# Kernel optimization log

Measured on AMD Instinct MI355X. Metric: run time of the kernel, lower is better.

The kernel has to match this reference:

```python
import jax, jax.numpy as jnp
import numpy as np
from jax import lax

B, D, H = 32768, 128, 256
N_ITER = 20


def setup_inputs() -> dict:
    key = jax.random.key(0)
    ks = jax.random.split(key, 7)
    return {
        "r": jax.random.normal(ks[0], (B, D), dtype=jnp.float32),
        "s": jax.random.normal(ks[1], (B, 1), dtype=jnp.float32),
        "pivot": jax.random.normal(ks[2], (D,), dtype=jnp.float32),
        "W1": jax.random.normal(ks[3], (D, H), dtype=jnp.float32) * 0.1,
        "b1": jax.random.normal(ks[4], (H,), dtype=jnp.float32) * 0.1,
        "w2": jax.random.normal(ks[5], (H,), dtype=jnp.float32) * 0.1,
        "b2": jax.random.normal(ks[6], (1,), dtype=jnp.float32) * 0.1,
        "n_iter": N_ITER,
    }


def _omega_step(x, W1, b1, w2, b2):
    # scalar implicit field omega evaluated on [B, D] points -> positive step in (0, 0.1)
    h = jnp.tanh(x @ W1 + b1)                      # [B, H]
    return 0.05 * (1.0 + jnp.tanh(h @ w2 + b2[0]))  # [B]


def reference(r, s, pivot, W1, b1, w2, b2, n_iter):
    # normalize ray directions; norm is detached in the original (stop_gradient)
    norm_of_x = jnp.linalg.norm(r, axis=1, keepdims=True)  # [B, 1]
    r_norm = r / lax.stop_gradient(norm_of_x)              # [B, D]

    # 20-step sphere-tracing-style ray marching along r_norm from pivot
    def step(alpha, _):
        x = pivot[None, :] + alpha[:, None] * r_norm       # [B, D]
        return alpha + _omega_step(x, W1, b1, w2, b2), None

    alpha0 = jnp.zeros((r.shape[0],), dtype=r.dtype)
    res_alpha, _ = lax.scan(step, alpha0, None, length=n_iter)  # [B]

    scale = jax.nn.sigmoid(s) * res_alpha[:, None]         # [B, 1]
    res_x = pivot[None, :] + scale * r_norm                # [B, D]
    return res_x
```

## Files before the change

### kernel.cpp

```cpp
#include <hip/hip_runtime.h>

#define DIM 128
#define HID 256
#define K2LE 2.885390081777927f
#define NTILES 16
#define RPB 32
#define BFPAD 136

typedef __attribute__((ext_vector_type(8))) short bf16x8;
typedef __attribute__((ext_vector_type(4))) float f32x4;

__device__ __forceinline__ unsigned short f2bf(float f) {
    union { float f; unsigned u; } x; x.f = f;
    unsigned r = x.u + 0x7fffu + ((x.u >> 16) & 1u);
    return (unsigned short)(r >> 16);
}

__device__ __forceinline__ float sigmoid_fast(float x) {
    float t = __builtin_amdgcn_exp2f(-x * 1.4426950408889634f);
    return __builtin_amdgcn_rcpf(1.0f + t);
}

__device__ __forceinline__ float row16_allreduce(float x) {
    int t;
    t = __builtin_amdgcn_update_dpp(0, __float_as_int(x), 0xB1, 0xf, 0xf, true);
    x += __int_as_float(t);
    t = __builtin_amdgcn_update_dpp(0, __float_as_int(x), 0x4E, 0xf, 0xf, true);
    x += __int_as_float(t);
    t = __builtin_amdgcn_update_dpp(0, __float_as_int(x), 0x124, 0xf, 0xf, true);
    x += __int_as_float(t);
    t = __builtin_amdgcn_update_dpp(0, __float_as_int(x), 0x128, 0xf, 0xf, true);
    x += __int_as_float(t);
    return x;
}

__global__ void k_prep(const float* __restrict__ pivot,
                       const float* __restrict__ W1,
                       const float* __restrict__ b1,
                       float* __restrict__ c2,
                       uint4* __restrict__ W1f) {
    const int tid = threadIdx.x;
    if (blockIdx.x == 0) {
        float a = b1[tid];
#pragma unroll 8
        for (int d = 0; d < DIM; ++d) a = fmaf(pivot[d], W1[d * HID + tid], a);
        c2[tid] = K2LE * a;
    }
    const int e  = blockIdx.x * 256 + tid;
    const int m  = e & 15;
    const int q  = (e >> 4) & 3;
    const int kk = (e >> 6) & 3;
    const int nt = e >> 8;
    const int n  = nt * 16 + m;
    const int k0 = kk * 32 + q * 8;
    unsigned w[4];
#pragma unroll
    for (int p = 0; p < 4; ++p) {
        unsigned lo = f2bf(W1[(k0 + 2 * p    ) * HID + n] * K2LE);
        unsigned hi = f2bf(W1[(k0 + 2 * p + 1) * HID + n] * K2LE);
        w[p] = lo | (hi << 16);
    }
    W1f[e] = make_uint4(w[0], w[1], w[2], w[3]);
}

__global__ __launch_bounds__(256, 4) void k_main(
    const float* __restrict__ r,
    const float* __restrict__ s,
    const float* __restrict__ pivot,
    const float* __restrict__ w2,
    const float* __restrict__ b2,
    const int* __restrict__ n_iter_p,
    const float* __restrict__ c2,
    const uint4* __restrict__ W1f,
    float* __restrict__ out)
{
    __shared__ unsigned short rnbf[RPB][BFPAD];
    __shared__ float rnf[RPB][DIM];
    __shared__ float alpha_s[RPB];

    const int tid  = threadIdx.x;
    const int lane = tid & 63;
    const int wave = tid >> 6;
    const int pr   = wave >> 1;
    const int par  = wave & 1;
    const int m    = lane & 15;
    const int q    = lane >> 4;
    const int rowblk = blockIdx.x * RPB;
    const int n_iter = *n_iter_p;

#pragma unroll
    for (int t = 0; t < 8; ++t) {
        const int lr = wave * 8 + t;
        float2 v = *(const float2*)&r[(rowblk + lr) * DIM + lane * 2];
        float ss = v.x * v.x + v.y * v.y;
#pragma unroll
        for (int msk = 32; msk >= 1; msk >>= 1) ss += __shfl_xor(ss, msk, 64);
        float inv = __builtin_amdgcn_rsqf(ss);
        float2 rn; rn.x = v.x * inv; rn.y = v.y * inv;
        *(float2*)&rnf[lr][lane * 2] = rn;
        unsigned pack = (unsigned)f2bf(rn.x) | ((unsigned)f2bf(rn.y) << 16);
        *(unsigned*)&rnbf[lr][lane * 2] = pack;
    }
    __syncthreads();

    bf16x8 afrag[4];
#pragma unroll
    for (int kk = 0; kk < 4; ++kk)
        afrag[kk] = *(const bf16x8*)&rnbf[pr * 16 + m][kk * 32 + q * 8];

    const bf16x8* __restrict__ wf = (const bf16x8*)W1f;
    const int fb = q * 16 + m;
    float gA[NTILES], gB[NTILES];
#pragma unroll
    for (int nt = 0; nt < NTILES; ++nt) {
        f32x4 a = {0.f, 0.f, 0.f, 0.f};
#pragma unroll
        for (int kk = 0; kk < 4; ++kk)
            a = __builtin_amdgcn_mfma_f32_16x16x32_bf16(
                    afrag[kk], wf[nt * 256 + kk * 64 + fb], a, 0, 0, 0);
        gA[nt] = a[par * 2 + 0];
        gB[nt] = a[par * 2 + 1];
    }

    float w2f[NTILES], c2f[NTILES];
#pragma unroll
    for (int nt = 0; nt < NTILES; ++nt) {
        w2f[nt] = w2[nt * 16 + m];
        c2f[nt] = c2[nt * 16 + m];
    }
    float S = 0.f;
#pragma unroll
    for (int nt = 0; nt < NTILES; ++nt) S += w2f[nt];
    S = row16_allreduce(S);
    const float C0 = K2LE * (S + b2[0]);

    float alphaA = 0.f, alphaB = 0.f;
    for (int it = 0; it < n_iter; ++it) {
        float pA = 0.f, pB = 0.f;
#pragma unroll
        for (int nt = 0; nt < NTILES; ++nt) {
            float uA = __builtin_amdgcn_rcpf(__builtin_amdgcn_exp2f(fmaf(alphaA, gA[nt], c2f[nt])) + 1.0f);
            float uB = __builtin_amdgcn_rcpf(__builtin_amdgcn_exp2f(fmaf(alphaB, gB[nt], c2f[nt])) + 1.0f);
            pA = fmaf(w2f[nt], uA, pA);
            pB = fmaf(w2f[nt], uB, pB);
        }
        pA = row16_allreduce(pA);
        pB = row16_allreduce(pB);
        float vA = __builtin_amdgcn_rcpf(__builtin_amdgcn_exp2f(fmaf(-2.0f * K2LE, pA, C0)) + 1.0f);
        float vB = __builtin_amdgcn_rcpf(__builtin_amdgcn_exp2f(fmaf(-2.0f * K2LE, pB, C0)) + 1.0f);
        alphaA += fmaf(-0.1f, vA, 0.1f);
        alphaB += fmaf(-0.1f, vB, 0.1f);
    }

    if (m == 0) {
        alpha_s[pr * 16 + q * 4 + par * 2 + 0] = alphaA;
        alpha_s[pr * 16 + q * 4 + par * 2 + 1] = alphaB;
    }
    __syncthreads();

    const float2 pv = *(const float2*)&pivot[lane * 2];
#pragma unroll
    for (int t = 0; t < 8; ++t) {
        const int lr  = wave * 8 + t;
        const int row = rowblk + lr;
        const float scale = sigmoid_fast(s[row]) * alpha_s[lr];
        float2 rn = *(const float2*)&rnf[lr][lane * 2];
        float2 o;
        o.x = fmaf(scale, rn.x, pv.x);
        o.y = fmaf(scale, rn.y, pv.y);
        *(float2*)&out[row * DIM + lane * 2] = o;
    }
}

extern "C" void kernel_launch(void* const* d_in, const int* in_sizes, int n_in,
                              void* d_out, int out_size, void* d_ws, size_t ws_size,
                              hipStream_t stream) {
    const float* r      = (const float*)d_in[0];
    const float* s      = (const float*)d_in[1];
    const float* pivot  = (const float*)d_in[2];
    const float* W1     = (const float*)d_in[3];
    const float* b1     = (const float*)d_in[4];
    const float* w2     = (const float*)d_in[5];
    const float* b2     = (const float*)d_in[6];
    const int*   n_iter = (const int*)d_in[7];
    float* out = (float*)d_out;

    float* c2  = (float*)d_ws;
    uint4* W1f = (uint4*)((char*)d_ws + 4096);

    const int B = in_sizes[0] / DIM;

    k_prep<<<16, 256, 0, stream>>>(pivot, W1, b1, c2, W1f);
    k_main<<<B / RPB, 256, 0, stream>>>(r, s, pivot, w2, b2, n_iter, c2, W1f, out);
}
```

Measured before the change: 131.1 us.

## Split fused kernel into GEMM and march kernels via bf16 workspace buffers

Splits the fused kernel into a GEMM kernel and a march kernel. The GEMM kernel computes the per-ray projection g = rn·W1 with MFMA and writes it to workspace as bf16, along with the normalized rays in bf16. The march kernel then runs the 20-iteration loop with one ray per 16 lanes and fewer registers, which allows higher occupancy (launch bounds 8). The aim is to stop the low-occupancy fused kernel from bottlenecking on transcendental latency. In exchange it adds about 24 MB of global traffic and two extra rounds of bf16 rounding: on g, and on the normalized direction used in the output. A fallback to the fused kernel is kept in case the workspace is too small.

```diff
diff --git a/kernel.cpp b/kernel.cpp
--- a/kernel.cpp
+++ b/kernel.cpp
@@ -4,7 +4,6 @@
 #define HID 256
 #define K2LE 2.885390081777927f
 #define NTILES 16
-#define RPB 32
 #define BFPAD 136
 
 typedef __attribute__((ext_vector_type(8))) short bf16x8;
@@ -15,6 +14,8 @@
     unsigned r = x.u + 0x7fffu + ((x.u >> 16) & 1u);
     return (unsigned short)(r >> 16);
 }
+__device__ __forceinline__ float bflo(unsigned u) { return __uint_as_float(u << 16); }
+__device__ __forceinline__ float bfhi(unsigned u) { return __uint_as_float(u & 0xffff0000u); }
 
 __device__ __forceinline__ float sigmoid_fast(float x) {
     float t = __builtin_amdgcn_exp2f(-x * 1.4426950408889634f);
@@ -37,14 +38,21 @@
 __global__ void k_prep(const float* __restrict__ pivot,
                        const float* __restrict__ W1,
                        const float* __restrict__ b1,
+                       const float* __restrict__ w2,
                        float* __restrict__ c2,
+                       float* __restrict__ c2p,
+                       float* __restrict__ w2p,
                        uint4* __restrict__ W1f) {
     const int tid = threadIdx.x;
     if (blockIdx.x == 0) {
         float a = b1[tid];
 #pragma unroll 8
         for (int d = 0; d < DIM; ++d) a = fmaf(pivot[d], W1[d * HID + tid], a);
-        c2[tid] = K2LE * a;
+        float cv = K2LE * a;
+        c2[tid] = cv;
+        const int pidx = (tid & 15) * 16 + (tid >> 4);
+        c2p[pidx] = cv;
+        w2p[pidx] = w2[tid];
     }
     const int e  = blockIdx.x * 256 + tid;
     const int m  = e & 15;
@@ -63,20 +71,148 @@
     W1f[e] = make_uint4(w[0], w[1], w[2], w[3]);
 }
 
-__global__ __launch_bounds__(256, 4) void k_main(
+__global__ __launch_bounds__(256, 4) void k_gemm(
     const float* __restrict__ r,
+    const uint4* __restrict__ W1f,
+    unsigned* __restrict__ rn_g,
+    uint4* __restrict__ g_buf)
+{
+    __shared__ unsigned short rnbf[64][BFPAD];
+
+    const int tid  = threadIdx.x;
+    const int lane = tid & 63;
+    const int wave = tid >> 6;
+    const int m    = lane & 15;
+    const int q    = lane >> 4;
+    const int rowb = blockIdx.x * 64 + wave * 16;
+
+#pragma unroll 4
+    for (int t = 0; t < 16; ++t) {
+        const int row = rowb + t;
+        float2 v = *(const float2*)&r[row * DIM + lane * 2];
+        float ss = v.x * v.x + v.y * v.y;
+#pragma unroll
+        for (int msk = 32; msk >= 1; msk >>= 1) ss += __shfl_xor(ss, msk, 64);
+        float inv = __builtin_amdgcn_rsqf(ss);
+        unsigned pack = (unsigned)f2bf(v.x * inv) | ((unsigned)f2bf(v.y * inv) << 16);
+        *(unsigned*)&rnbf[wave * 16 + t][lane * 2] = pack;
+        rn_g[row * 64 + lane] = pack;
+    }
+
+    bf16x8 afrag[4];
+#pragma unroll
+    for (int kk = 0; kk < 4; ++kk)
+        afrag[kk] = *(const bf16x8*)&rnbf[wave * 16 + m][kk * 32 + q * 8];
+
+    const bf16x8* __restrict__ wf = (const bf16x8*)W1f;
+    const int fb = q * 16 + m;
+    unsigned pk[4][8];
+#pragma unroll
+    for (int nt = 0; nt < NTILES; ++nt) {
+        f32x4 a = {0.f, 0.f, 0.f, 0.f};
+#pragma unroll
+        for (int kk = 0; kk < 4; ++kk)
+            a = __builtin_amdgcn_mfma_f32_16x16x32_bf16(
+                    afrag[kk], wf[nt * 256 + kk * 64 + fb], a, 0, 0, 0);
+#pragma unroll
+        for (int reg = 0; reg < 4; ++reg) {
+            unsigned h = f2bf(a[reg]);
+            if (nt & 1) pk[reg][nt >> 1] |= (h << 16);
+            else        pk[reg][nt >> 1]  = h;
+        }
+    }
+#pragma unroll
+    for (int reg = 0; reg < 4; ++reg) {
+        const int ray = rowb + q * 4 + reg;
+        uint4* p = g_buf + ray * 32 + m * 2;
+        p[0] = make_uint4(pk[reg][0], pk[reg][1], pk[reg][2], pk[reg][3]);
+        p[1] = make_uint4(pk[reg][4], pk[reg][5], pk[reg][6], pk[reg][7]);
+    }
+}
+
+__global__ __launch_bounds__(256, 8) void k_march(
+    const uint4* __restrict__ g_buf,
+    const uint4* __restrict__ rn_g,
     const float* __restrict__ s,
     const float* __restrict__ pivot,
-    const float* __restrict__ w2,
+    const float* __restrict__ c2p,
+    const float* __restrict__ w2p,
     const float* __restrict__ b2,
     const int* __restrict__ n_iter_p,
-    const float* __restrict__ c2,
-    const uint4* __restrict__ W1f,
     float* __restrict__ out)
 {
-    __shared__ unsigned short rnbf[RPB][BFPAD];
-    __shared__ float rnf[RPB][DIM];
-    __shared__ float alpha_s[RPB];
+    const int tid  = threadIdx.x;
+    const int lane = tid & 63;
+    const int wave = tid >> 6;
+    const int m    = lane & 15;
+    const int q    = lane >> 4;
+    const int ray  = blockIdx.x * 16 + wave * 4 + q;
+    const int n_iter = *n_iter_p;
+
+    uint4 ga = g_buf[ray * 32 + m * 2];
+    uint4 gb = g_buf[ray * 32 + m * 2 + 1];
+    float g[16];
+    g[0]=bflo(ga.x); g[1]=bfhi(ga.x); g[2]=bflo(ga.y); g[3]=bfhi(ga.y);
+    g[4]=bflo(ga.z); g[5]=bfhi(ga.z); g[6]=bflo(ga.w); g[7]=bfhi(ga.w);
+    g[8]=bflo(gb.x); g[9]=bfhi(gb.x); g[10]=bflo(gb.y); g[11]=bfhi(gb.y);
+    g[12]=bflo(gb.z); g[13]=bfhi(gb.z); g[14]=bflo(gb.w); g[15]=bfhi(gb.w);
+
+    float c[16], w[16];
+#pragma unroll
+    for (int i = 0; i < 4; ++i) {
+        float4 cv = *(const float4*)(c2p + m * 16 + i * 4);
+        float4 wv = *(const float4*)(w2p + m * 16 + i * 4);
+        c[4*i]=cv.x; c[4*i+1]=cv.y; c[4*i+2]=cv.z; c[4*i+3]=cv.w;
+        w[4*i]=wv.x; w[4*i+1]=wv.y; w[4*i+2]=wv.z; w[4*i+3]=wv.w;
+    }
+    float S = 0.f;
+#pragma unroll
+    for (int i = 0; i < 16; ++i) S += w[i];
+    S = row16_allreduce(S);
+    const float C0 = K2LE * (S + b2[0]);
+
+    float alpha = 0.f;
+    for (int it = 0; it < n_iter; ++it) {
+        float p = 0.f;
+#pragma unroll
+        for (int i = 0; i < 16; ++i) {
+            float u = __builtin_amdgcn_rcpf(
+                __builtin_amdgcn_exp2f(fmaf(alpha, g[i], c[i])) + 1.0f);
+            p = fmaf(w[i], u, p);
+        }
+        p = row16_allreduce(p);
+        float v = __builtin_amdgcn_rcpf(
+            __builtin_amdgcn_exp2f(fmaf(-2.0f * K2LE, p, C0)) + 1.0f);
+        alpha += fmaf(-0.1f, v, 0.1f);
+    }
+
+    const float sc = sigmoid_fast(s[ray]) * alpha;
+    uint4 rl = rn_g[ray * 16 + m];
+    float4 pv0 = *(const float4*)(pivot + m * 8);
+    float4 pv1 = *(const float4*)(pivot + m * 8 + 4);
+    float4 o0, o1;
+    o0.x = fmaf(sc, bflo(rl.x), pv0.x);
+    o0.y = fmaf(sc, bfhi(rl.x), pv0.y);
+    o0.z = fmaf(sc, bflo(rl.y), pv0.z);
+    o0.w = fmaf(sc, bfhi(rl.y), pv0.w);
+    o1.x = fmaf(sc, bflo(rl.z), pv1.x);
+    o1.y = fmaf(sc, bfhi(rl.z), pv1.y);
+    o1.z = fmaf(sc, bflo(rl.w), pv1.z);
+    o1.w = fmaf(sc, bfhi(rl.w), pv1.w);
+    *(float4*)(out + ray * DIM + m * 8)     = o0;
+    *(float4*)(out + ray * DIM + m * 8 + 4) = o1;
+}
+
+__global__ __launch_bounds__(256, 4) void k_main_fused(
+    const float* __restrict__ r, const float* __restrict__ s,
+    const float* __restrict__ pivot, const float* __restrict__ w2,
+    const float* __restrict__ b2, const int* __restrict__ n_iter_p,
+    const float* __restrict__ c2, const uint4* __restrict__ W1f,
+    float* __restrict__ out)
+{
+    __shared__ unsigned short rnbf[32][BFPAD];
+    __shared__ float rnf[32][DIM];
+    __shared__ float alpha_s[32];
 
     const int tid  = threadIdx.x;
     const int lane = tid & 63;
@@ -85,7 +221,7 @@
     const int par  = wave & 1;
     const int m    = lane & 15;
     const int q    = lane >> 4;
-    const int rowblk = blockIdx.x * RPB;
+    const int rowblk = blockIdx.x * 32;
     const int n_iter = *n_iter_p;
 
 #pragma unroll
@@ -121,7 +257,6 @@
         gA[nt] = a[par * 2 + 0];
         gB[nt] = a[par * 2 + 1];
     }
-
     float w2f[NTILES], c2f[NTILES];
 #pragma unroll
     for (int nt = 0; nt < NTILES; ++nt) {
@@ -151,7 +286,6 @@
         alphaA += fmaf(-0.1f, vA, 0.1f);
         alphaB += fmaf(-0.1f, vB, 0.1f);
     }
-
     if (m == 0) {
         alpha_s[pr * 16 + q * 4 + par * 2 + 0] = alphaA;
         alpha_s[pr * 16 + q * 4 + par * 2 + 1] = alphaB;
@@ -185,11 +319,25 @@
     const int*   n_iter = (const int*)d_in[7];
     float* out = (float*)d_out;
 
-    float* c2  = (float*)d_ws;
-    uint4* W1f = (uint4*)((char*)d_ws + 4096);
-
     const int B = in_sizes[0] / DIM;
 
-    k_prep<<<16, 256, 0, stream>>>(pivot, W1, b1, c2, W1f);
-    k_main<<<B / RPB, 256, 0, stream>>>(r, s, pivot, w2, b2, n_iter, c2, W1f, out);
-}
+    char* ws = (char*)d_ws;
+    float* c2   = (float*)(ws);
+    float* c2p  = (float*)(ws + 1024);
+    float* w2p  = (float*)(ws + 2048);
+    uint4* W1f  = (uint4*)(ws + 4096);
+    uint4* g_buf = (uint4*)(ws + 69632);
+    unsigned* rn_g = (unsigned*)(ws + 69632 + (size_t)B * 512);
+
+    const size_t need = 69632 + (size_t)B * 768;
+
+    k_prep<<<16, 256, 0, stream>>>(pivot, W1, b1, w2, c2, c2p, w2p, W1f);
+    if (ws_size >= need) {
+        k_gemm<<<B / 64, 256, 0, stream>>>(r, W1f, rn_g, g_buf);
+        k_march<<<B / 16, 256, 0, stream>>>(g_buf, (const uint4*)rn_g, s, pivot,
+                                            c2p, w2p, b2, n_iter, out);
+    } else {
+        k_main_fused<<<B / 32, 256, 0, stream>>>(r, s, pivot, w2, b2, n_iter,
+                                                 c2, W1f, out);
+    }
+}
```

Result: slower. 142.8 us (+8.9%).

## Split hidden-tile MFMA across waves and map one ray per 16-lane group

Applied to the files above, without the earlier changes.

Each block now handles 16 rays instead of 32. Each wave computes only 4 of the 16 hidden tiles of the projection with MFMA, and the waves exchange the results through shared memory, so the projection is no longer recomputed redundantly in every wave. In the march loop each 16-lane group owns one ray instead of each lane carrying two, which lowers register pressure and allows a launch bound of 8 blocks instead of 4. The c2/w2 constants are pre-permuted in the prep kernel so they can be read with vector loads. The fp32 normalized-ray copy is dropped and the output is rebuilt from bf16-rounded directions, which adds numerical error to the result.

```diff
diff --git a/kernel.cpp b/kernel.cpp
--- a/kernel.cpp
+++ b/kernel.cpp
@@ -4,8 +4,6 @@
 #define HID 256
 #define K2LE 2.885390081777927f
 #define NTILES 16
-#define RPB 32
-#define BFPAD 136
 
 typedef __attribute__((ext_vector_type(8))) short bf16x8;
 typedef __attribute__((ext_vector_type(4))) float f32x4;
@@ -15,6 +13,8 @@
     unsigned r = x.u + 0x7fffu + ((x.u >> 16) & 1u);
     return (unsigned short)(r >> 16);
 }
+__device__ __forceinline__ float bflo(unsigned u) { return __uint_as_float(u << 16); }
+__device__ __forceinline__ float bfhi(unsigned u) { return __uint_as_float(u & 0xffff0000u); }
 
 __device__ __forceinline__ float sigmoid_fast(float x) {
     float t = __builtin_amdgcn_exp2f(-x * 1.4426950408889634f);
@@ -37,14 +37,18 @@
 __global__ void k_prep(const float* __restrict__ pivot,
                        const float* __restrict__ W1,
                        const float* __restrict__ b1,
-                       float* __restrict__ c2,
+                       const float* __restrict__ w2,
+                       float* __restrict__ c2p,
+                       float* __restrict__ w2p,
                        uint4* __restrict__ W1f) {
     const int tid = threadIdx.x;
     if (blockIdx.x == 0) {
         float a = b1[tid];
 #pragma unroll 8
         for (int d = 0; d < DIM; ++d) a = fmaf(pivot[d], W1[d * HID + tid], a);
-        c2[tid] = K2LE * a;
+        const int pidx = (tid & 15) * 16 + (tid >> 4);
+        c2p[pidx] = K2LE * a;
+        w2p[pidx] = w2[tid];
     }
     const int e  = blockIdx.x * 256 + tid;
     const int m  = e & 15;
@@ -63,113 +67,109 @@
     W1f[e] = make_uint4(w[0], w[1], w[2], w[3]);
 }
 
-__global__ __launch_bounds__(256, 4) void k_main(
+__global__ __launch_bounds__(256, 8) void k_main(
     const float* __restrict__ r,
     const float* __restrict__ s,
     const float* __restrict__ pivot,
-    const float* __restrict__ w2,
+    const float* __restrict__ c2p,
+    const float* __restrict__ w2p,
     const float* __restrict__ b2,
     const int* __restrict__ n_iter_p,
-    const float* __restrict__ c2,
     const uint4* __restrict__ W1f,
     float* __restrict__ out)
 {
-    __shared__ unsigned short rnbf[RPB][BFPAD];
-    __shared__ float rnf[RPB][DIM];
-    __shared__ float alpha_s[RPB];
+    __shared__ unsigned short rnbf[16][128];
+    __shared__ float g_x[16][HID];
 
-    const int tid  = threadIdx.x;
-    const int lane = tid & 63;
-    const int wave = tid >> 6;
-    const int pr   = wave >> 1;
-    const int par  = wave & 1;
-    const int m    = lane & 15;
-    const int q    = lane >> 4;
-    const int rowblk = blockIdx.x * RPB;
+    const int tid   = threadIdx.x;
+    const int lane  = tid & 63;
+    const int wave  = tid >> 6;
+    const int m     = lane & 15;
+    const int q     = lane >> 4;
+    const int ray_l = wave * 4 + q;
+    const int ray_g = blockIdx.x * 16 + ray_l;
     const int n_iter = *n_iter_p;
 
-#pragma unroll
-    for (int t = 0; t < 8; ++t) {
-        const int lr = wave * 8 + t;
-        float2 v = *(const float2*)&r[(rowblk + lr) * DIM + lane * 2];
-        float ss = v.x * v.x + v.y * v.y;
-#pragma unroll
-        for (int msk = 32; msk >= 1; msk >>= 1) ss += __shfl_xor(ss, msk, 64);
-        float inv = __builtin_amdgcn_rsqf(ss);
-        float2 rn; rn.x = v.x * inv; rn.y = v.y * inv;
-        *(float2*)&rnf[lr][lane * 2] = rn;
-        unsigned pack = (unsigned)f2bf(rn.x) | ((unsigned)f2bf(rn.y) << 16);
-        *(unsigned*)&rnbf[lr][lane * 2] = pack;
-    }
+    float4 v0 = *(const float4*)&r[ray_g * DIM + m * 8];
+    float4 v1 = *(const float4*)&r[ray_g * DIM + m * 8 + 4];
+    float ss = v0.x*v0.x + v0.y*v0.y + v0.z*v0.z + v0.w*v0.w
+             + v1.x*v1.x + v1.y*v1.y + v1.z*v1.z + v1.w*v1.w;
+    ss = row16_allreduce(ss);
+    const float inv = __builtin_amdgcn_rsqf(ss);
+    unsigned p0 = (unsigned)f2bf(v0.x*inv) | ((unsigned)f2bf(v0.y*inv) << 16);
+    unsigned p1 = (unsigned)f2bf(v0.z*inv) | ((unsigned)f2bf(v0.w*inv) << 16);
+    unsigned p2 = (unsigned)f2bf(v1.x*inv) | ((unsigned)f2bf(v1.y*inv) << 16);
+    unsigned p3 = (unsigned)f2bf(v1.z*inv) | ((unsigned)f2bf(v1.w*inv) << 16);
+    *(uint4*)&rnbf[ray_l][m * 8] = make_uint4(p0, p1, p2, p3);
     __syncthreads();
 
     bf16x8 afrag[4];
 #pragma unroll
     for (int kk = 0; kk < 4; ++kk)
-        afrag[kk] = *(const bf16x8*)&rnbf[pr * 16 + m][kk * 32 + q * 8];
+        afrag[kk] = *(const bf16x8*)&rnbf[m][kk * 32 + q * 8];
 
     const bf16x8* __restrict__ wf = (const bf16x8*)W1f;
     const int fb = q * 16 + m;
-    float gA[NTILES], gB[NTILES];
 #pragma unroll
-    for (int nt = 0; nt < NTILES; ++nt) {
+    for (int t = 0; t < 4; ++t) {
+        const int nt = wave * 4 + t;
         f32x4 a = {0.f, 0.f, 0.f, 0.f};
 #pragma unroll
         for (int kk = 0; kk < 4; ++kk)
             a = __builtin_amdgcn_mfma_f32_16x16x32_bf16(
                     afrag[kk], wf[nt * 256 + kk * 64 + fb], a, 0, 0, 0);
-        gA[nt] = a[par * 2 + 0];
-        gB[nt] = a[par * 2 + 1];
+#pragma unroll
+        for (int r4 = 0; r4 < 4; ++r4)
+            g_x[q * 4 + r4][nt * 16 + m] = a[r4];
     }
+    __syncthreads();
 
-    float w2f[NTILES], c2f[NTILES];
+    float g[16], c[16], w[16];
 #pragma unroll
-    for (int nt = 0; nt < NTILES; ++nt) {
-        w2f[nt] = w2[nt * 16 + m];
-        c2f[nt] = c2[nt * 16 + m];
+    for (int i = 0; i < 16; ++i) g[i] = g_x[ray_l][i * 16 + m];
+#pragma unroll
+    for (int i = 0; i < 4; ++i) {
+        float4 cv = *(const float4*)(c2p + m * 16 + i * 4);
+        float4 wv = *(const float4*)(w2p + m * 16 + i * 4);
+        c[4*i]=cv.x; c[4*i+1]=cv.y; c[4*i+2]=cv.z; c[4*i+3]=cv.w;
+        w[4*i]=wv.x; w[4*i+1]=wv.y; w[4*i+2]=wv.z; w[4*i+3]=wv.w;
     }
     float S = 0.f;
 #pragma unroll
-    for (int nt = 0; nt < NTILES; ++nt) S += w2f[nt];
+    for (int i = 0; i < 16; ++i) S += w[i];
     S = row16_allreduce(S);
     const float C0 = K2LE * (S + b2[0]);
 
-    float alphaA = 0.f, alphaB = 0.f;
+    float alpha = 0.f;
     for (int it = 0; it < n_iter; ++it) {
-        float pA = 0.f, pB = 0.f;
+        float p = 0.f;
 #pragma unroll
-        for (int nt = 0; nt < NTILES; ++nt) {
-            float uA = __builtin_amdgcn_rcpf(__builtin_amdgcn_exp2f(fmaf(alphaA, gA[nt], c2f[nt])) + 1.0f);
-            float uB = __builtin_amdgcn_rcpf(__builtin_amdgcn_exp2f(fmaf(alphaB, gB[nt], c2f[nt])) + 1.0f);
-            pA = fmaf(w2f[nt], uA, pA);
-            pB = fmaf(w2f[nt], uB, pB);
+        for (int i = 0; i < 16; ++i) {
+            float u = __builtin_amdgcn_rcpf(
+                __builtin_amdgcn_exp2f(fmaf(alpha, g[i], c[i])) + 1.0f);
+            p = fmaf(w[i], u, p);
         }
-        pA = row16_allreduce(pA);
-        pB = row16_allreduce(pB);
-        float vA = __builtin_amdgcn_rcpf(__builtin_amdgcn_exp2f(fmaf(-2.0f * K2LE, pA, C0)) + 1.0f);
-        float vB = __builtin_amdgcn_rcpf(__builtin_amdgcn_exp2f(fmaf(-2.0f * K2LE, pB, C0)) + 1.0f);
-        alphaA += fmaf(-0.1f, vA, 0.1f);
-        alphaB += fmaf(-0.1f, vB, 0.1f);
+        p = row16_allreduce(p);
+        float v = __builtin_amdgcn_rcpf(
+            __builtin_amdgcn_exp2f(fmaf(-2.0f * K2LE, p, C0)) + 1.0f);
+        alpha += fmaf(-0.1f, v, 0.1f);
     }
 
-    if (m == 0) {
-        alpha_s[pr * 16 + q * 4 + par * 2 + 0] = alphaA;
-        alpha_s[pr * 16 + q * 4 + par * 2 + 1] = alphaB;
-    }
-    __syncthreads();
-
-    const float2 pv = *(const float2*)&pivot[lane * 2];
-#pragma unroll
-    for (int t = 0; t < 8; ++t) {
-        const int lr  = wave * 8 + t;
-        const int row = rowblk + lr;
-        const float scale = sigmoid_fast(s[row]) * alpha_s[lr];
-        float2 rn = *(const float2*)&rnf[lr][lane * 2];
-        float2 o;
-        o.x = fmaf(scale, rn.x, pv.x);
-        o.y = fmaf(scale, rn.y, pv.y);
-        *(float2*)&out[row * DIM + lane * 2] = o;
-    }
+    const float sc = sigmoid_fast(s[ray_g]) * alpha;
+    uint4 rl = *(const uint4*)&rnbf[ray_l][m * 8];
+    float4 pv0 = *(const float4*)(pivot + m * 8);
+    float4 pv1 = *(const float4*)(pivot + m * 8 + 4);
+    float4 o0, o1;
+    o0.x = fmaf(sc, bflo(rl.x), pv0.x);
+    o0.y = fmaf(sc, bfhi(rl.x), pv0.y);
+    o0.z = fmaf(sc, bflo(rl.y), pv0.z);
+    o0.w = fmaf(sc, bfhi(rl.y), pv0.w);
+    o1.x = fmaf(sc, bflo(rl.z), pv1.x);
+    o1.y = fmaf(sc, bfhi(rl.z), pv1.y);
+    o1.z = fmaf(sc, bflo(rl.w), pv1.z);
+    o1.w = fmaf(sc, bfhi(rl.w), pv1.w);
+    *(float4*)(out + ray_g * DIM + m * 8)     = o0;
+    *(float4*)(out + ray_g * DIM + m * 8 + 4) = o1;
 }
 
 extern "C" void kernel_launch(void* const* d_in, const int* in_sizes, int n_in,
@@ -185,11 +185,14 @@
     const int*   n_iter = (const int*)d_in[7];
     float* out = (float*)d_out;
 
-    float* c2  = (float*)d_ws;
-    uint4* W1f = (uint4*)((char*)d_ws + 4096);
-
     const int B = in_sizes[0] / DIM;
 
-    k_prep<<<16, 256, 0, stream>>>(pivot, W1, b1, c2, W1f);
-    k_main<<<B / RPB, 256, 0, stream>>>(r, s, pivot, w2, b2, n_iter, c2, W1f, out);
+    char* ws = (char*)d_ws;
+    float* c2p = (float*)(ws);
+    float* w2p = (float*)(ws + 1024);
+    uint4* W1f = (uint4*)(ws + 4096);
+
+    k_prep<<<16, 256, 0, stream>>>(pivot, W1, b1, w2, c2p, w2p, W1f);
+    k_main<<<B / 16, 256, 0, stream>>>(r, s, pivot, c2p, w2p, b2, n_iter,
+                                       W1f, out);
 }
```

After: 123.4 us. 1.06x faster.
